# Performance work log

Hardware: AMD Instinct MI355X
Metric: run time of the kernel (lower is better)

The kernel has to match this reference:

```python
import jax, jax.numpy as jnp
import numpy as np

N = 50000
E = 800000
IN_C = 128
HID = 64
HEADS = 4
OUT_C = 64


def setup_inputs() -> dict:
    key = jax.random.key(0)
    ks = jax.random.split(key, 20)
    s = 0.05
    inp = {
        "x": jax.random.normal(ks[0], (N, IN_C), dtype=jnp.float32),
        "edge_index": jax.random.randint(ks[1], (2, E), 0, N, dtype=jnp.int64),
        # layer 0: in=128 -> heads=4, C=64
        "W0": jax.random.normal(ks[2], (IN_C, HEADS * HID), jnp.float32) * s,
        "a0s": jax.random.normal(ks[3], (HEADS, HID), jnp.float32) * s,
        "a0d": jax.random.normal(ks[4], (HEADS, HID), jnp.float32) * s,
        "b0": jnp.zeros((HEADS * HID,), jnp.float32),
        # layer 1: 256 -> heads=4, C=64
        "W1": jax.random.normal(ks[5], (HEADS * HID, HEADS * HID), jnp.float32) * s,
        "a1s": jax.random.normal(ks[6], (HEADS, HID), jnp.float32) * s,
        "a1d": jax.random.normal(ks[7], (HEADS, HID), jnp.float32) * s,
        "b1": jnp.zeros((HEADS * HID,), jnp.float32),
        # layer 2: 256 -> heads=1, C=64
        "W2": jax.random.normal(ks[8], (HEADS * HID, HID), jnp.float32) * s,
        "a2s": jax.random.normal(ks[9], (1, HID), jnp.float32) * s,
        "a2d": jax.random.normal(ks[10], (1, HID), jnp.float32) * s,
        "b2": jnp.zeros((HID,), jnp.float32),
        # prediction head: Linear(64 -> 64)
        "hw": jax.random.normal(ks[11], (HID, OUT_C), jnp.float32) * s,
        "hb": jnp.zeros((OUT_C,), jnp.float32),
    }
    return inp


def gat_conv(x, src, dst, W, a_s, a_d, b, heads, n_nodes):
    # x: [N, F_in]; returns [N, heads*C]
    C = a_s.shape[1]
    h = (x @ W).reshape(n_nodes, heads, C)          # [N,H,C]
    alpha_s = jnp.sum(h * a_s, axis=-1)             # [N,H]
    alpha_d = jnp.sum(h * a_d, axis=-1)             # [N,H]
    e = jax.nn.leaky_relu(alpha_s[src] + alpha_d[dst], negative_slope=0.2)  # [E,H]
    m = jax.ops.segment_max(e, dst, num_segments=n_nodes)                  # per-dst max
    ex = jnp.exp(e - m[dst])
    denom = jax.ops.segment_sum(ex, dst, num_segments=n_nodes)
    alpha = ex / (denom[dst] + 1e-16)               # [E,H]
    out = jax.ops.segment_sum(alpha[:, :, None] * h[src], dst, num_segments=n_nodes)
    return out.reshape(n_nodes, heads * C) + b


def reference(x, edge_index, W0, a0s, a0d, b0, W1, a1s, a1d, b1, W2, a2s, a2d, b2, hw, hb):
    n = x.shape[0]
    # PyG GATConv default add_self_loops=True
    loop = jnp.arange(n, dtype=edge_index.dtype)
    src = jnp.concatenate([edge_index[0], loop])
    dst = jnp.concatenate([edge_index[1], loop])

    h = gat_conv(x, src, dst, W0, a0s, a0d, b0, HEADS, n)
    h = jax.nn.relu(h)
    h = gat_conv(h, src, dst, W1, a1s, a1d, b1, HEADS, n)
    h = jax.nn.relu(h)
    h = gat_conv(h, src, dst, W2, a2s, a2d, b2, 1, n)
    # batch is None -> mean over all nodes, keepdim
    g = jnp.mean(h, axis=0, keepdims=True)          # [1, HID]
    return g @ hw + hb                               # [1, OUT_C]
```

## Files before the change

kernel.cpp:

```cpp
#include <hip/hip_runtime.h>
#include <hip/hip_bf16.h>
#include <cstddef>

#define NN 50000
#define EE 800000
#define NB ((NN + 255) / 256)

typedef __attribute__((ext_vector_type(8))) short short8;
typedef __attribute__((ext_vector_type(4))) float f32x4;

#define GLB __attribute__((address_space(1)))
#define LDS __attribute__((address_space(3)))

__device__ __forceinline__ float leaky(float x) { return x >= 0.f ? x : 0.2f * x; }
__device__ __forceinline__ float bf2f(unsigned short u) {
  return __uint_as_float(((unsigned int)u) << 16);
}
__device__ __forceinline__ float bflo(unsigned int v) { return __uint_as_float(v << 16); }
__device__ __forceinline__ float bfhi(unsigned int v) { return __uint_as_float(v & 0xFFFF0000u); }
__device__ __forceinline__ unsigned short f2bf(float f) {
  __hip_bfloat16 b = __float2bfloat16(f);
  return __builtin_bit_cast(unsigned short, b);
}
__device__ __forceinline__ float selh(float4 v, int h) {
  float a = (h & 1) ? v.y : v.x;
  float b = (h & 1) ? v.w : v.z;
  return (h & 2) ? b : a;
}
__device__ __forceinline__ void accum8(float a, uint4 v, float* acc) {
  acc[0] += a * bflo(v.x); acc[1] += a * bfhi(v.x);
  acc[2] += a * bflo(v.y); acc[3] += a * bfhi(v.y);
  acc[4] += a * bflo(v.z); acc[5] += a * bfhi(v.z);
  acc[6] += a * bflo(v.w); acc[7] += a * bfhi(v.w);
}

__global__ __launch_bounds__(256) void gemm_bf16_k(const unsigned short* __restrict__ A,
                                                   const unsigned short* __restrict__ Bt,
                                                   unsigned short* __restrict__ Cb,
                                                   int K, int Nfull,
                                                   const float* __restrict__ a_s,
                                                   const float* __restrict__ a_d,
                                                   float* __restrict__ als,
                                                   float* __restrict__ ald,
                                                   float* __restrict__ selfex) {
  __shared__ __align__(16) unsigned short As[128 * 32];
  __shared__ __align__(16) unsigned short Bs[64 * 32];
  const int tid = threadIdx.x;
  const int lane = tid & 63;
  const int w = tid >> 6;
  const int bm = blockIdx.x * 128;
  const int bn = blockIdx.y * 64;
  const int quad = lane >> 4;
  const int l16 = lane & 15;
  const int lrow = lane >> 2;
  const int lseg = lane & 3;
  f32x4 acc[2][4] = {};
  for (int kc = 0; kc < K; kc += 32) {
#pragma unroll
    for (int c = 0; c < 2; ++c) {
      int row = w * 32 + c * 16 + lrow;
      int g = lseg ^ ((row >> 2) & 3);
      int sr = bm + row; if (sr >= NN) sr = NN - 1;
      const unsigned short* gp = A + (size_t)sr * K + kc + g * 8;
      __builtin_amdgcn_global_load_lds((const GLB void*)gp,
                                       (LDS void*)&As[(w * 32 + c * 16) * 32], 16, 0, 0);
    }
    {
      int row = w * 16 + lrow;
      int g = lseg ^ ((row >> 2) & 3);
      const unsigned short* gp = Bt + (size_t)(bn + row) * K + kc + g * 8;
      __builtin_amdgcn_global_load_lds((const GLB void*)gp,
                                       (LDS void*)&Bs[(w * 16) * 32], 16, 0, 0);
    }
    __syncthreads();
    const int ra0 = w * 32 + l16;
    const int ra1 = ra0 + 16;
    short8 afr0 = *(const short8*)&As[ra0 * 32 + ((quad ^ ((ra0 >> 2) & 3)) << 3)];
    short8 afr1 = *(const short8*)&As[ra1 * 32 + ((quad ^ ((ra1 >> 2) & 3)) << 3)];
#pragma unroll
    for (int nt = 0; nt < 4; ++nt) {
      int rb = nt * 16 + l16;
      short8 bfr = *(const short8*)&Bs[rb * 32 + ((quad ^ ((rb >> 2) & 3)) << 3)];
      acc[0][nt] = __builtin_amdgcn_mfma_f32_16x16x32_bf16(afr0, bfr, acc[0][nt], 0, 0, 0);
      acc[1][nt] = __builtin_amdgcn_mfma_f32_16x16x32_bf16(afr1, bfr, acc[1][nt], 0, 0, 0);
    }
    __syncthreads();
  }
  const int head = bn >> 6;
  const int Hmul = Nfull >> 6;
  float vs[2][4] = {};
  float vd[2][4] = {};
#pragma unroll
  for (int nt = 0; nt < 4; ++nt) {
    const float asv = a_s[head * 64 + nt * 16 + l16];
    const float adv = a_d[head * 64 + nt * 16 + l16];
#pragma unroll
    for (int mt = 0; mt < 2; ++mt)
#pragma unroll
      for (int reg = 0; reg < 4; ++reg) {
        unsigned short c = f2bf(acc[mt][nt][reg]);
        int r = bm + w * 32 + mt * 16 + quad * 4 + reg;
        if (r < NN) Cb[(size_t)r * Nfull + bn + nt * 16 + l16] = c;
        float hv = bf2f(c);
        vs[mt][reg] += hv * asv;
        vd[mt][reg] += hv * adv;
      }
  }
#pragma unroll
  for (int off = 1; off < 16; off <<= 1) {
#pragma unroll
    for (int mt = 0; mt < 2; ++mt)
#pragma unroll
      for (int reg = 0; reg < 4; ++reg) {
        vs[mt][reg] += __shfl_xor(vs[mt][reg], off, 64);
        vd[mt][reg] += __shfl_xor(vd[mt][reg], off, 64);
      }
  }
  if (l16 == 0) {
#pragma unroll
    for (int mt = 0; mt < 2; ++mt)
#pragma unroll
      for (int reg = 0; reg < 4; ++reg) {
        int r = bm + w * 32 + mt * 16 + quad * 4 + reg;
        if (r < NN) {
          als[(size_t)r * Hmul + head] = vs[mt][reg];
          ald[(size_t)r * Hmul + head] = vd[mt][reg];
          selfex[(size_t)r * Hmul + head] = __expf(leaky(vs[mt][reg] + vd[mt][reg]));
        }
      }
  }
}

__global__ __launch_bounds__(256) void hist_k(const int* __restrict__ ei, int* deg) {
  int i = blockIdx.x * 256 + threadIdx.x;
  if (i < EE) atomicAdd(&deg[ei[EE + i]], 1);
}

__global__ __launch_bounds__(256) void scan1_k(const int* __restrict__ deg,
                                               int* __restrict__ incl,
                                               int* __restrict__ partial) {
  __shared__ int s[256];
  int t = threadIdx.x;
  int i = blockIdx.x * 256 + t;
  int v = (i < NN) ? deg[i] : 0;
  s[t] = v;
  __syncthreads();
  for (int off = 1; off < 256; off <<= 1) {
    int u = (t >= off) ? s[t - off] : 0;
    __syncthreads();
    s[t] += u;
    __syncthreads();
  }
  if (i < NN) incl[i] = s[t];
  if (t == 255) partial[blockIdx.x] = s[255];
}

__global__ __launch_bounds__(256) void scan23_k(const int* __restrict__ deg,
                                                const int* __restrict__ incl,
                                                const int* __restrict__ partial,
                                                int* __restrict__ rowptr,
                                                int* __restrict__ cursor) {
  __shared__ int s[256];
  __shared__ int ex[256];
  int t = threadIdx.x;
  int v = (t < NB) ? partial[t] : 0;
  s[t] = v;
  __syncthreads();
  for (int off = 1; off < 256; off <<= 1) {
    int u = (t >= off) ? s[t - off] : 0;
    __syncthreads();
    s[t] += u;
    __syncthreads();
  }
  ex[t] = s[t] - v;
  __syncthreads();
  int base = ex[blockIdx.x];
  int i = blockIdx.x * 256 + t;
  if (i < NN) {
    int r = base + incl[i] - deg[i];
    rowptr[i] = r;
    cursor[i] = r;
  }
}

__global__ __launch_bounds__(256) void scatter_k(const int* __restrict__ ei,
                                                 int* __restrict__ cursor,
                                                 int* __restrict__ csr_src) {
  int i = blockIdx.x * 256 + threadIdx.x;
  if (i >= EE) return;
  int d = ei[EE + i];
  int p = atomicAdd(&cursor[d], 1);
  csr_src[p] = ei[i];
}

__global__ __launch_bounds__(256) void aggr4c_k(const int* __restrict__ rowptr,
                                                const int* __restrict__ deg,
                                                const int* __restrict__ csr_src,
                                                const float* __restrict__ als,
                                                const float* __restrict__ ald,
                                                const float* __restrict__ selfex,
                                                const uint4* __restrict__ hb4,
                                                const float* __restrict__ bias,
                                                uint4* __restrict__ out4) {
  const int dst = blockIdx.x * 4 + (threadIdx.x >> 6);
  const int lane = threadIdx.x & 63;
  const int slot = lane >> 4;
  const int l16 = lane & 15;
  const int head = l16 >> 2;
  const int rs = rowptr[dst];
  const int dg = deg[dst];
  const float aldv = ald[dst * 4 + head];

  float acc[16] = {};
  float dsum = 0.f;
  if (slot == 0) {
    float a = selfex[dst * 4 + head];
    dsum += a;
    uint4 v0 = hb4[(size_t)dst * 32 + l16 * 2];
    uint4 v1 = hb4[(size_t)dst * 32 + l16 * 2 + 1];
    accum8(a, v0, acc);
    accum8(a, v1, acc + 8);
  }
  int j = slot;
  for (; j + 4 < dg; j += 8) {
    int s0 = csr_src[rs + j];
    int s1 = csr_src[rs + j + 4];
    float e0 = als[s0 * 4 + head];
    float e1 = als[s1 * 4 + head];
    uint4 va0 = hb4[(size_t)s0 * 32 + l16 * 2];
    uint4 vb0 = hb4[(size_t)s0 * 32 + l16 * 2 + 1];
    uint4 va1 = hb4[(size_t)s1 * 32 + l16 * 2];
    uint4 vb1 = hb4[(size_t)s1 * 32 + l16 * 2 + 1];
    float a0 = __expf(leaky(e0 + aldv));
    float a1 = __expf(leaky(e1 + aldv));
    dsum += a0 + a1;
    accum8(a0, va0, acc);
    accum8(a0, vb0, acc + 8);
    accum8(a1, va1, acc);
    accum8(a1, vb1, acc + 8);
  }
  for (; j < dg; j += 4) {
    int s0 = csr_src[rs + j];
    float e0 = als[s0 * 4 + head];
    uint4 va0 = hb4[(size_t)s0 * 32 + l16 * 2];
    uint4 vb0 = hb4[(size_t)s0 * 32 + l16 * 2 + 1];
    float a0 = __expf(leaky(e0 + aldv));
    dsum += a0;
    accum8(a0, va0, acc);
    accum8(a0, vb0, acc + 8);
  }
#pragma unroll
  for (int k = 0; k < 16; ++k) {
    acc[k] += __shfl_xor(acc[k], 16, 64);
    acc[k] += __shfl_xor(acc[k], 32, 64);
  }
  dsum += __shfl_xor(dsum, 16, 64);
  dsum += __shfl_xor(dsum, 32, 64);
  if (slot == 0) {
    const float inv = 1.f / (dsum + 1e-16f);
    const float* bz = bias + l16 * 16;
    uint4 o0, o1;
    float c0, c1;
    c0 = fmaxf(acc[0] * inv + bz[0], 0.f);   c1 = fmaxf(acc[1] * inv + bz[1], 0.f);
    o0.x = ((unsigned int)f2bf(c1) << 16) | f2bf(c0);
    c0 = fmaxf(acc[2] * inv + bz[2], 0.f);   c1 = fmaxf(acc[3] * inv + bz[3], 0.f);
    o0.y = ((unsigned int)f2bf(c1) << 16) | f2bf(c0);
    c0 = fmaxf(acc[4] * inv + bz[4], 0.f);   c1 = fmaxf(acc[5] * inv + bz[5], 0.f);
    o0.z = ((unsigned int)f2bf(c1) << 16) | f2bf(c0);
    c0 = fmaxf(acc[6] * inv + bz[6], 0.f);   c1 = fmaxf(acc[7] * inv + bz[7], 0.f);
    o0.w = ((unsigned int)f2bf(c1) << 16) | f2bf(c0);
    c0 = fmaxf(acc[8] * inv + bz[8], 0.f);   c1 = fmaxf(acc[9] * inv + bz[9], 0.f);
    o1.x = ((unsigned int)f2bf(c1) << 16) | f2bf(c0);
    c0 = fmaxf(acc[10] * inv + bz[10], 0.f); c1 = fmaxf(acc[11] * inv + bz[11], 0.f);
    o1.y = ((unsigned int)f2bf(c1) << 16) | f2bf(c0);
    c0 = fmaxf(acc[12] * inv + bz[12], 0.f); c1 = fmaxf(acc[13] * inv + bz[13], 0.f);
    o1.z = ((unsigned int)f2bf(c1) << 16) | f2bf(c0);
    c0 = fmaxf(acc[14] * inv + bz[14], 0.f); c1 = fmaxf(acc[15] * inv + bz[15], 0.f);
    o1.w = ((unsigned int)f2bf(c1) << 16) | f2bf(c0);
    out4[(size_t)dst * 32 + l16 * 2] = o0;
    out4[(size_t)dst * 32 + l16 * 2 + 1] = o1;
  }
}

__global__ __launch_bounds__(256) void aggr1c_k(const int* __restrict__ rowptr,
                                                const int* __restrict__ deg,
                                                const int* __restrict__ csr_src,
                                                const float* __restrict__ als,
                                                const float* __restrict__ ald,
                                                const float* __restrict__ selfex,
                                                const uint4* __restrict__ hb4,
                                                const float* __restrict__ bias,
                                                float* __restrict__ out) {
  const int dst = blockIdx.x * 4 + (threadIdx.x >> 6);
  const int lane = threadIdx.x & 63;
  const int slot = lane >> 3;
  const int c8 = lane & 7;
  const int rs = rowptr[dst];
  const int dg = deg[dst];
  const float aldv = ald[dst];

  float acc[8] = {};
  float dsum = 0.f;
  if (slot == 0) {
    float a = selfex[dst];
    dsum += a;
    uint4 v = hb4[(size_t)dst * 8 + c8];
    accum8(a, v, acc);
  }
  for (int j = slot; j < dg; j += 8) {
    int s = csr_src[rs + j];
    float e = als[s];
    uint4 v = hb4[(size_t)s * 8 + c8];
    float a = __expf(leaky(e + aldv));
    dsum += a;
    accum8(a, v, acc);
  }
#pragma unroll
  for (int k = 0; k < 8; ++k) {
    acc[k] += __shfl_xor(acc[k], 8, 64);
    acc[k] += __shfl_xor(acc[k], 16, 64);
    acc[k] += __shfl_xor(acc[k], 32, 64);
  }
  dsum += __shfl_xor(dsum, 8, 64);
  dsum += __shfl_xor(dsum, 16, 64);
  dsum += __shfl_xor(dsum, 32, 64);
  if (slot == 0) {
    const float inv = 1.f / (dsum + 1e-16f);
    const float4 bz0 = *(const float4*)(bias + c8 * 8);
    const float4 bz1 = *(const float4*)(bias + c8 * 8 + 4);
    float4 o0 = make_float4(acc[0] * inv + bz0.x, acc[1] * inv + bz0.y,
                            acc[2] * inv + bz0.z, acc[3] * inv + bz0.w);
    float4 o1 = make_float4(acc[4] * inv + bz1.x, acc[5] * inv + bz1.y,
                            acc[6] * inv + bz1.z, acc[7] * inv + bz1.w);
    *(float4*)(out + (size_t)dst * 64 + c8 * 8) = o0;
    *(float4*)(out + (size_t)dst * 64 + c8 * 8 + 4) = o1;
  }
}

__global__ __launch_bounds__(256) void prep_k(const float2* __restrict__ x2,
                                              unsigned int* __restrict__ xb_u,
                                              const float* __restrict__ W0,
                                              unsigned short* __restrict__ W0t,
                                              const float* __restrict__ W1,
                                              unsigned short* __restrict__ W1t,
                                              const float* __restrict__ W2,
                                              unsigned short* __restrict__ W2t,
                                              int* __restrict__ deg,
                                              float* __restrict__ g) {
  int bid = blockIdx.x;
  int tid = threadIdx.x;
  if (bid < 12500) {
    int i = bid * 256 + tid;
    float2 v = x2[i];
    xb_u[i] = ((unsigned int)f2bf(v.y) << 16) | f2bf(v.x);
    return;
  }
  if (bid < 12948) {
    int r = (bid - 12500) * 256 + tid;
    if (r < 32768) {
      int n = r >> 7, k = r & 127;
      W0t[n * 128 + k] = f2bf(W0[k * 256 + n]);
    } else if (r < 98304) {
      int rr = r - 32768;
      int n = rr >> 8, k = rr & 255;
      W1t[n * 256 + k] = f2bf(W1[k * 256 + n]);
    } else {
      int rr = r - 98304;
      int n = rr >> 8, k = rr & 255;
      W2t[n * 256 + k] = f2bf(W2[k * 64 + n]);
    }
    return;
  }
  if (bid < 13144) {
    int i = (bid - 12948) * 256 + tid;
    if (i < NN) deg[i] = 0;
    return;
  }
  if (tid < 68) g[tid] = 0.f;
}

__global__ __launch_bounds__(256) void colsum_head_k(const float* __restrict__ h2,
                                                     float* __restrict__ g,
                                                     unsigned int* __restrict__ cnt,
                                                     const float* __restrict__ hw,
                                                     const float* __restrict__ hb,
                                                     float* __restrict__ out) {
  __shared__ float s[256];
  __shared__ float sg[64];
  __shared__ unsigned int sdone;
  int tid = threadIdx.x;
  int c = tid & 63, rg = tid >> 6;
  float acc = 0.f;
  for (int n = blockIdx.x * 4 + rg; n < NN; n += gridDim.x * 4)
    acc += h2[n * 64 + c];
  s[tid] = acc;
  __syncthreads();
  if (tid < 64) atomicAdd(&g[c], s[c] + s[64 + c] + s[128 + c] + s[192 + c]);
  __threadfence();
  __syncthreads();
  if (tid == 0) sdone = atomicAdd(cnt, 1);
  __syncthreads();
  if (sdone != gridDim.x - 1) return;
  if (tid < 64) sg[tid] = atomicAdd(&g[tid], 0.f);
  __syncthreads();
  if (tid < 64) {
    const float invN = 1.0f / (float)NN;
    float a2 = hb[tid];
#pragma unroll 8
    for (int cc = 0; cc < 64; ++cc) a2 += sg[cc] * invN * hw[cc * 64 + tid];
    out[tid] = a2;
  }
}

extern "C" void kernel_launch(void* const* d_in, const int* in_sizes, int n_in,
                              void* d_out, int out_size, void* d_ws, size_t ws_size,
                              hipStream_t stream) {
  const float* x   = (const float*)d_in[0];
  const int*   ei  = (const int*)d_in[1];
  const float* W0  = (const float*)d_in[2];
  const float* a0s = (const float*)d_in[3];
  const float* a0d = (const float*)d_in[4];
  const float* b0  = (const float*)d_in[5];
  const float* W1  = (const float*)d_in[6];
  const float* a1s = (const float*)d_in[7];
  const float* a1d = (const float*)d_in[8];
  const float* b1  = (const float*)d_in[9];
  const float* W2  = (const float*)d_in[10];
  const float* a2s = (const float*)d_in[11];
  const float* a2d = (const float*)d_in[12];
  const float* b2  = (const float*)d_in[13];
  const float* hw  = (const float*)d_in[14];
  const float* hb  = (const float*)d_in[15];
  float* out = (float*)d_out;

  char* w = (char*)d_ws;
  unsigned short* xb   = (unsigned short*)w; w += (size_t)NN * 128 * 2;
  unsigned short* bufG = (unsigned short*)w; w += (size_t)NN * 256 * 2;
  unsigned short* bufA = (unsigned short*)w; w += (size_t)NN * 256 * 2;
  float* bufF = (float*)w;                   w += (size_t)NN * 64 * 4;
  unsigned short* W0t = (unsigned short*)w;  w += 256 * 128 * 2;
  unsigned short* W1t = (unsigned short*)w;  w += 256 * 256 * 2;
  unsigned short* W2t = (unsigned short*)w;  w += 64 * 256 * 2;
  float* als  = (float*)w;    w += (size_t)NN * 4 * 4;
  float* ald  = (float*)w;    w += (size_t)NN * 4 * 4;
  float* sfx  = (float*)w;    w += (size_t)NN * 4 * 4;
  int* deg     = (int*)w;     w += (size_t)NN * 4;
  int* rowptr  = (int*)w;     w += (size_t)NN * 4;
  int* cursor  = (int*)w;     w += (size_t)NN * 4;
  int* incl    = (int*)w;     w += (size_t)NN * 4;
  int* partial = (int*)w;     w += 256 * 4;
  int* csr_src = (int*)w;     w += (size_t)EE * 4;
  float* g    = (float*)w;    w += 256;

  prep_k<<<13145, 256, 0, stream>>>((const float2*)x, (unsigned int*)xb,
                                    W0, W0t, W1, W1t, W2, W2t, deg, g);

  hist_k<<<(EE + 255) / 256, 256, 0, stream>>>(ei, deg);
  scan1_k<<<NB, 256, 0, stream>>>(deg, incl, partial);
  scan23_k<<<NB, 256, 0, stream>>>(deg, incl, partial, rowptr, cursor);
  scatter_k<<<(EE + 255) / 256, 256, 0, stream>>>(ei, cursor, csr_src);

  const int GX = (NN + 127) / 128;
  const int GA = NN / 4;

  auto layer4 = [&](const unsigned short* in, int K, const unsigned short* Wt,
                    const float* a_s, const float* a_d, const float* bias,
                    unsigned short* hbuf, unsigned short* obuf) {
    gemm_bf16_k<<<dim3(GX, 4), 256, 0, stream>>>(in, Wt, hbuf, K, 256,
                                                 a_s, a_d, als, ald, sfx);
    aggr4c_k<<<GA, 256, 0, stream>>>(rowptr, deg, csr_src, als, ald, sfx,
                                     (const uint4*)hbuf, bias, (uint4*)obuf);
  };

  layer4(xb, 128, W0t, a0s, a0d, b0, bufG, bufA);
  layer4(bufA, 256, W1t, a1s, a1d, b1, bufG, bufA);

  gemm_bf16_k<<<dim3(GX, 1), 256, 0, stream>>>(bufA, W2t, bufG, 256, 64,
                                               a2s, a2d, als, ald, sfx);
  aggr1c_k<<<GA, 256, 0, stream>>>(rowptr, deg, csr_src, als, ald, sfx,
                                   (const uint4*)bufG, b2, bufF);

  colsum_head_k<<<256, 256, 0, stream>>>(bufF, g, (unsigned int*)(g + 64), hw, hb, out);
}
```

Measured before the change: 441.7 us.

## Stage CSR indices in LDS and software-pipeline neighbor gathers in GAT aggregation

Each block of 4 destination nodes first copies its contiguous slice of CSR source indices (up to 1024) into shared memory, so the per-edge index loads hit LDS instead of global memory. The neighbor loop is restructured into a masked, software-pipelined loop: the next iteration's attention logits and feature rows are loaded before the current ones are accumulated, which hides gather latency. Launch bounds now request 8 blocks per multiprocessor. In exchange there is a block-wide barrier, extra register pressure from the double-buffered uint4 values, and redundant self-row loads on non-zero slots.

```diff
diff --git a/kernel.cpp b/kernel.cpp
--- a/kernel.cpp
+++ b/kernel.cpp
@@ -193,61 +193,84 @@
   csr_src[p] = ei[i];
 }
 
-__global__ __launch_bounds__(256) void aggr4c_k(const int* __restrict__ rowptr,
-                                                const int* __restrict__ deg,
-                                                const int* __restrict__ csr_src,
-                                                const float* __restrict__ als,
-                                                const float* __restrict__ ald,
-                                                const float* __restrict__ selfex,
-                                                const uint4* __restrict__ hb4,
-                                                const float* __restrict__ bias,
-                                                uint4* __restrict__ out4) {
-  const int dst = blockIdx.x * 4 + (threadIdx.x >> 6);
-  const int lane = threadIdx.x & 63;
+__global__ __launch_bounds__(256, 8) void aggr4c_k(const int* __restrict__ rowptr,
+                                                   const int* __restrict__ deg,
+                                                   const int* __restrict__ csr_src,
+                                                   const float* __restrict__ als,
+                                                   const float* __restrict__ ald,
+                                                   const float* __restrict__ selfex,
+                                                   const uint4* __restrict__ hb4,
+                                                   const float* __restrict__ bias,
+                                                   uint4* __restrict__ out4) {
+  __shared__ int sidx[1024];
+  const int b4 = blockIdx.x * 4;
+  const int tid = threadIdx.x;
+  const int rbase = rowptr[b4];
+  const int rend = rowptr[b4 + 3] + deg[b4 + 3];
+  const int total = rend - rbase;
+  const int tmax = total < 1024 ? total : 1024;
+  for (int t = tid; t < tmax; t += 256) sidx[t] = csr_src[rbase + t];
+
+  const int dst = b4 + (tid >> 6);
+  const int lane = tid & 63;
   const int slot = lane >> 4;
   const int l16 = lane & 15;
   const int head = l16 >> 2;
-  const int rs = rowptr[dst];
+  const int rs = rowptr[dst] - rbase;
   const int dg = deg[dst];
   const float aldv = ald[dst * 4 + head];
+  const uint4* hp = hb4 + l16 * 2;
+
+  const float a_self = (slot == 0) ? selfex[dst * 4 + head] : 0.f;
+  uint4 v0s = hp[(size_t)dst * 32];
+  uint4 v1s = hp[(size_t)dst * 32 + 1];
+  __syncthreads();
 
   float acc[16] = {};
-  float dsum = 0.f;
-  if (slot == 0) {
-    float a = selfex[dst * 4 + head];
-    dsum += a;
-    uint4 v0 = hb4[(size_t)dst * 32 + l16 * 2];
-    uint4 v1 = hb4[(size_t)dst * 32 + l16 * 2 + 1];
-    accum8(a, v0, acc);
-    accum8(a, v1, acc + 8);
-  }
-  int j = slot;
-  for (; j + 4 < dg; j += 8) {
-    int s0 = csr_src[rs + j];
-    int s1 = csr_src[rs + j + 4];
+  float dsum = a_self;
+  accum8(a_self, v0s, acc);
+  accum8(a_self, v1s, acc + 8);
+
+  const int nst = (dg + 7) >> 3;
+  float p0 = 0.f, p1 = 0.f;
+  uint4 va0 = {}, vb0 = {}, va1 = {}, vb1 = {};
+  if (nst > 0) {
+    int j0 = slot, j1 = slot + 4;
+    bool m0 = j0 < dg, m1 = j1 < dg;
+    int i0 = m0 ? rs + j0 : rs;
+    int i1 = m1 ? rs + j1 : rs;
+    int s0 = (i0 < 1024) ? sidx[i0] : csr_src[rbase + i0];
+    int s1 = (i1 < 1024) ? sidx[i1] : csr_src[rbase + i1];
     float e0 = als[s0 * 4 + head];
     float e1 = als[s1 * 4 + head];
-    uint4 va0 = hb4[(size_t)s0 * 32 + l16 * 2];
-    uint4 vb0 = hb4[(size_t)s0 * 32 + l16 * 2 + 1];
-    uint4 va1 = hb4[(size_t)s1 * 32 + l16 * 2];
-    uint4 vb1 = hb4[(size_t)s1 * 32 + l16 * 2 + 1];
-    float a0 = __expf(leaky(e0 + aldv));
-    float a1 = __expf(leaky(e1 + aldv));
-    dsum += a0 + a1;
-    accum8(a0, va0, acc);
-    accum8(a0, vb0, acc + 8);
-    accum8(a1, va1, acc);
-    accum8(a1, vb1, acc + 8);
-  }
-  for (; j < dg; j += 4) {
-    int s0 = csr_src[rs + j];
+    va0 = hp[(size_t)s0 * 32]; vb0 = hp[(size_t)s0 * 32 + 1];
+    va1 = hp[(size_t)s1 * 32]; vb1 = hp[(size_t)s1 * 32 + 1];
+    p0 = m0 ? __expf(leaky(e0 + aldv)) : 0.f;
+    p1 = m1 ? __expf(leaky(e1 + aldv)) : 0.f;
+  }
+  for (int t = 1; t < nst; ++t) {
+    int j0 = t * 8 + slot, j1 = j0 + 4;
+    bool m0 = j0 < dg, m1 = j1 < dg;
+    int i0 = m0 ? rs + j0 : rs;
+    int i1 = m1 ? rs + j1 : rs;
+    int s0 = (i0 < 1024) ? sidx[i0] : csr_src[rbase + i0];
+    int s1 = (i1 < 1024) ? sidx[i1] : csr_src[rbase + i1];
     float e0 = als[s0 * 4 + head];
-    uint4 va0 = hb4[(size_t)s0 * 32 + l16 * 2];
-    uint4 vb0 = hb4[(size_t)s0 * 32 + l16 * 2 + 1];
-    float a0 = __expf(leaky(e0 + aldv));
-    dsum += a0;
-    accum8(a0, va0, acc);
-    accum8(a0, vb0, acc + 8);
+    float e1 = als[s1 * 4 + head];
+    uint4 wa0 = hp[(size_t)s0 * 32], wb0 = hp[(size_t)s0 * 32 + 1];
+    uint4 wa1 = hp[(size_t)s1 * 32], wb1 = hp[(size_t)s1 * 32 + 1];
+    float q0 = m0 ? __expf(leaky(e0 + aldv)) : 0.f;
+    float q1 = m1 ? __expf(leaky(e1 + aldv)) : 0.f;
+    dsum += p0 + p1;
+    accum8(p0, va0, acc); accum8(p0, vb0, acc + 8);
+    accum8(p1, va1, acc); accum8(p1, vb1, acc + 8);
+    va0 = wa0; vb0 = wb0; va1 = wa1; vb1 = wb1;
+    p0 = q0; p1 = q1;
+  }
+  if (nst > 0) {
+    dsum += p0 + p1;
+    accum8(p0, va0, acc); accum8(p0, vb0, acc + 8);
+    accum8(p1, va1, acc); accum8(p1, vb1, acc + 8);
   }
 #pragma unroll
   for (int k = 0; k < 16; ++k) {
@@ -282,38 +305,69 @@
   }
 }
 
-__global__ __launch_bounds__(256) void aggr1c_k(const int* __restrict__ rowptr,
-                                                const int* __restrict__ deg,
-                                                const int* __restrict__ csr_src,
-                                                const float* __restrict__ als,
-                                                const float* __restrict__ ald,
-                                                const float* __restrict__ selfex,
-                                                const uint4* __restrict__ hb4,
-                                                const float* __restrict__ bias,
-                                                float* __restrict__ out) {
-  const int dst = blockIdx.x * 4 + (threadIdx.x >> 6);
-  const int lane = threadIdx.x & 63;
+__global__ __launch_bounds__(256, 8) void aggr1c_k(const int* __restrict__ rowptr,
+                                                   const int* __restrict__ deg,
+                                                   const int* __restrict__ csr_src,
+                                                   const float* __restrict__ als,
+                                                   const float* __restrict__ ald,
+                                                   const float* __restrict__ selfex,
+                                                   const uint4* __restrict__ hb4,
+                                                   const float* __restrict__ bias,
+                                                   float* __restrict__ out) {
+  __shared__ int sidx[1024];
+  const int b4 = blockIdx.x * 4;
+  const int tid = threadIdx.x;
+  const int rbase = rowptr[b4];
+  const int rend = rowptr[b4 + 3] + deg[b4 + 3];
+  const int total = rend - rbase;
+  const int tmax = total < 1024 ? total : 1024;
+  for (int t = tid; t < tmax; t += 256) sidx[t] = csr_src[rbase + t];
+
+  const int dst = b4 + (tid >> 6);
+  const int lane = tid & 63;
   const int slot = lane >> 3;
   const int c8 = lane & 7;
-  const int rs = rowptr[dst];
+  const int rs = rowptr[dst] - rbase;
   const int dg = deg[dst];
   const float aldv = ald[dst];
+  const uint4* hp = hb4 + c8;
+
+  const float a_self = (slot == 0) ? selfex[dst] : 0.f;
+  uint4 vsl = hp[(size_t)dst * 8];
+  __syncthreads();
 
   float acc[8] = {};
-  float dsum = 0.f;
-  if (slot == 0) {
-    float a = selfex[dst];
-    dsum += a;
-    uint4 v = hb4[(size_t)dst * 8 + c8];
-    accum8(a, v, acc);
-  }
-  for (int j = slot; j < dg; j += 8) {
-    int s = csr_src[rs + j];
+  float dsum = a_self;
+  accum8(a_self, vsl, acc);
+
+  const int nst = (dg + 7) >> 3;
+  float p0 = 0.f;
+  uint4 va = {};
+  if (nst > 0) {
+    int j = slot;
+    bool m = j < dg;
+    int i = m ? rs + j : rs;
+    int s = (i < 1024) ? sidx[i] : csr_src[rbase + i];
     float e = als[s];
-    uint4 v = hb4[(size_t)s * 8 + c8];
-    float a = __expf(leaky(e + aldv));
-    dsum += a;
-    accum8(a, v, acc);
+    va = hp[(size_t)s * 8];
+    p0 = m ? __expf(leaky(e + aldv)) : 0.f;
+  }
+  for (int t = 1; t < nst; ++t) {
+    int j = t * 8 + slot;
+    bool m = j < dg;
+    int i = m ? rs + j : rs;
+    int s = (i < 1024) ? sidx[i] : csr_src[rbase + i];
+    float e = als[s];
+    uint4 wa = hp[(size_t)s * 8];
+    float q = m ? __expf(leaky(e + aldv)) : 0.f;
+    dsum += p0;
+    accum8(p0, va, acc);
+    va = wa;
+    p0 = q;
+  }
+  if (nst > 0) {
+    dsum += p0;
+    accum8(p0, va, acc);
   }
 #pragma unroll
   for (int k = 0; k < 8; ++k) {
```

After: 554.5 us. 25.5% more time.

## Add full-width 64x256 GEMM tile for 4-head layers with fused attention logits

Applied to the files above, without the earlier changes.

Adds a new GEMM kernel in which each block computes a 64-row by 256-column output tile, covering all four heads. Each A tile is loaded once instead of being re-read by four column blocks. The per-node source/destination attention logits and the self-loop exponential are computed in the epilogue from the full row. The trade-off is more accumulator registers per thread (16 MFMA tiles), a larger B tile in LDS, and fewer rows per block, which could lower occupancy.

```diff
diff --git a/kernel.cpp b/kernel.cpp
--- a/kernel.cpp
+++ b/kernel.cpp
@@ -22,16 +22,103 @@
   __hip_bfloat16 b = __float2bfloat16(f);
   return __builtin_bit_cast(unsigned short, b);
 }
-__device__ __forceinline__ float selh(float4 v, int h) {
-  float a = (h & 1) ? v.y : v.x;
-  float b = (h & 1) ? v.w : v.z;
-  return (h & 2) ? b : a;
-}
 __device__ __forceinline__ void accum8(float a, uint4 v, float* acc) {
   acc[0] += a * bflo(v.x); acc[1] += a * bfhi(v.x);
   acc[2] += a * bflo(v.y); acc[3] += a * bfhi(v.y);
   acc[4] += a * bflo(v.z); acc[5] += a * bfhi(v.z);
   acc[6] += a * bflo(v.w); acc[7] += a * bfhi(v.w);
+}
+
+__global__ __launch_bounds__(256) void gemm256_k(const unsigned short* __restrict__ A,
+                                                 const unsigned short* __restrict__ Bt,
+                                                 unsigned short* __restrict__ Cb,
+                                                 int K,
+                                                 const float* __restrict__ a_s,
+                                                 const float* __restrict__ a_d,
+                                                 float* __restrict__ als,
+                                                 float* __restrict__ ald,
+                                                 float* __restrict__ selfex) {
+  __shared__ __align__(16) unsigned short As[64 * 32];
+  __shared__ __align__(16) unsigned short Bs[256 * 32];
+  const int tid = threadIdx.x;
+  const int lane = tid & 63;
+  const int w = tid >> 6;
+  const int bm = blockIdx.x * 64;
+  const int quad = lane >> 4;
+  const int l16 = lane & 15;
+  const int lrow = lane >> 2;
+  const int lseg = lane & 3;
+  f32x4 acc[16] = {};
+  for (int kc = 0; kc < K; kc += 32) {
+    {
+      int row = w * 16 + lrow;
+      int g = lseg ^ ((row >> 2) & 3);
+      int sr = bm + row; if (sr >= NN) sr = NN - 1;
+      const unsigned short* gp = A + (size_t)sr * K + kc + g * 8;
+      __builtin_amdgcn_global_load_lds((const GLB void*)gp,
+                                       (LDS void*)&As[(w * 16) * 32], 16, 0, 0);
+    }
+#pragma unroll
+    for (int c = 0; c < 4; ++c) {
+      int row = w * 64 + c * 16 + lrow;
+      int g = lseg ^ ((row >> 2) & 3);
+      const unsigned short* gp = Bt + (size_t)row * K + kc + g * 8;
+      __builtin_amdgcn_global_load_lds((const GLB void*)gp,
+                                       (LDS void*)&Bs[(w * 64 + c * 16) * 32], 16, 0, 0);
+    }
+    __syncthreads();
+    const int ra = w * 16 + l16;
+    short8 afr = *(const short8*)&As[ra * 32 + ((quad ^ ((ra >> 2) & 3)) << 3)];
+#pragma unroll
+    for (int nt = 0; nt < 16; ++nt) {
+      int rb = nt * 16 + l16;
+      short8 bfr = *(const short8*)&Bs[rb * 32 + ((quad ^ ((rb >> 2) & 3)) << 3)];
+      acc[nt] = __builtin_amdgcn_mfma_f32_16x16x32_bf16(afr, bfr, acc[nt], 0, 0, 0);
+    }
+    __syncthreads();
+  }
+  float vs[4][4] = {};
+  float vd[4][4] = {};
+#pragma unroll
+  for (int nt = 0; nt < 16; ++nt) {
+    const int h = nt >> 2;
+    const float asv = a_s[h * 64 + (nt & 3) * 16 + l16];
+    const float adv = a_d[h * 64 + (nt & 3) * 16 + l16];
+#pragma unroll
+    for (int reg = 0; reg < 4; ++reg) {
+      unsigned short c = f2bf(acc[nt][reg]);
+      int r = bm + w * 16 + quad * 4 + reg;
+      if (r < NN) Cb[(size_t)r * 256 + nt * 16 + l16] = c;
+      float hv = bf2f(c);
+      vs[h][reg] += hv * asv;
+      vd[h][reg] += hv * adv;
+    }
+  }
+#pragma unroll
+  for (int off = 1; off < 16; off <<= 1) {
+#pragma unroll
+    for (int h = 0; h < 4; ++h)
+#pragma unroll
+      for (int reg = 0; reg < 4; ++reg) {
+        vs[h][reg] += __shfl_xor(vs[h][reg], off, 64);
+        vd[h][reg] += __shfl_xor(vd[h][reg], off, 64);
+      }
+  }
+  if (l16 == 0) {
+#pragma unroll
+    for (int reg = 0; reg < 4; ++reg) {
+      int r = bm + w * 16 + quad * 4 + reg;
+      if (r < NN) {
+        float4 fs = make_float4(vs[0][reg], vs[1][reg], vs[2][reg], vs[3][reg]);
+        float4 fd = make_float4(vd[0][reg], vd[1][reg], vd[2][reg], vd[3][reg]);
+        *(float4*)&als[(size_t)r * 4] = fs;
+        *(float4*)&ald[(size_t)r * 4] = fd;
+        float4 se = make_float4(__expf(leaky(fs.x + fd.x)), __expf(leaky(fs.y + fd.y)),
+                                __expf(leaky(fs.z + fd.z)), __expf(leaky(fs.w + fd.w)));
+        *(float4*)&selfex[(size_t)r * 4] = se;
+      }
+    }
+  }
 }
 
 __global__ __launch_bounds__(256) void gemm_bf16_k(const unsigned short* __restrict__ A,
@@ -461,13 +548,13 @@
   scatter_k<<<(EE + 255) / 256, 256, 0, stream>>>(ei, cursor, csr_src);
 
   const int GX = (NN + 127) / 128;
+  const int G64 = (NN + 63) / 64;
   const int GA = NN / 4;
 
   auto layer4 = [&](const unsigned short* in, int K, const unsigned short* Wt,
                     const float* a_s, const float* a_d, const float* bias,
                     unsigned short* hbuf, unsigned short* obuf) {
-    gemm_bf16_k<<<dim3(GX, 4), 256, 0, stream>>>(in, Wt, hbuf, K, 256,
-                                                 a_s, a_d, als, ald, sfx);
+    gemm256_k<<<G64, 256, 0, stream>>>(in, Wt, hbuf, K, a_s, a_d, als, ald, sfx);
     aggr4c_k<<<GA, 256, 0, stream>>>(rowptr, deg, csr_src, als, ald, sfx,
                                      (const uint4*)hbuf, bias, (uint4*)obuf);
   };
```

Result: no change. 433.5 us (-1.9%).
